# Kernel tuning notes

Hardware: AMD Instinct MI355X
Metric: run time of the kernel (lower is better)

## Reference

```python
import jax, jax.numpy as jnp
import numpy as np

B, CIN, HW = 32, 64, 56
K, KS, STRIDE, PAD = 128, 3, 1, 1


def setup_inputs() -> dict:
    key = jax.random.key(0)
    kx, kw, kb = jax.random.split(key, 3)
    x = jax.random.normal(kx, (B, CIN, HW, HW), dtype=jnp.float32)
    weight = jax.random.normal(kw, (K, CIN, KS, KS), dtype=jnp.float32)
    offset = jax.random.normal(kb, (K, 1, 1), dtype=jnp.float32)
    return {"x": x, "weight": weight, "offset": offset}


def reference(x, weight, offset):
    # conv2d (NCHW, OIHW) with stride/padding, then add per-kernel scalar offset.
    # Equivalent to the module's im2col (create_window_column_matrix) + matmul
    # + reshape, plus self.offset broadcast over (B, K, s, s).
    out = jax.lax.conv_general_dilated(
        x, weight,
        window_strides=(STRIDE, STRIDE),
        padding=[(PAD, PAD), (PAD, PAD)],
        dimension_numbers=("NCHW", "OIHW", "NCHW"),
    )
    return out + offset  # offset (K,1,1) broadcasts against (B,K,s,s)
```

## Files before the change

kernel.cpp:

```cpp
#include <hip/hip_runtime.h>
#include <hip/hip_bf16.h>

namespace {

using frag_t    = __attribute__((ext_vector_type(8))) short;
using f32x4     = __attribute__((ext_vector_type(4))) float;
using float4_t  = __attribute__((ext_vector_type(4))) float;

constexpr int BATCH = 32;
constexpr int CIN   = 64;
constexpr int HWD   = 56;
constexpr int KOUT  = 128;
constexpr int SP    = HWD * HWD;
constexpr int KD    = 9 * CIN;
constexpr int BN    = 64;
constexpr int HALO  = 57;
constexpr int NROWS = BN + 2 * HALO;
constexpr int NSTA  = 192;
constexpr int NTILES= SP / BN;
constexpr int NWG   = NTILES * BATCH;
constexpr int TT    = BATCH * (SP / 64);
constexpr int WB    = (KOUT * KD + 255) / 256;

__device__ inline unsigned short f2bf(float f) {
    __hip_bfloat16 h = __float2bfloat16(f);
    return __builtin_bit_cast(unsigned short, h);
}

__global__ __launch_bounds__(256)
void prep_kernel(const float* __restrict__ x, const float* __restrict__ w,
                 unsigned short* __restrict__ wpA, unsigned short* __restrict__ xT)
{
    if (blockIdx.x >= TT) {
        const int idx = (blockIdx.x - TT) * 256 + threadIdx.x;
        if (idx < KOUT * KD) {
            const int kout = idx / KD, kk = idx - kout * KD;
            const int kc = kk >> 5, e = kk & 31;
            const int t = kk >> 6, c = kk & 63;
            const int ky = t / 3, kx = t - ky * 3;
            wpA[(kc * KOUT + kout) * 32 + e] = f2bf(w[((kout * CIN + c) * 3 + ky) * 3 + kx]);
        }
        return;
    }
    __shared__ float ls[64][68];
    const int bb   = blockIdx.x / (SP / 64);
    const int tile = blockIdx.x - bb * (SP / 64);
    const int sp0  = tile * 64;
    const int tid  = threadIdx.x;
    const int cq   = tid >> 4;
    const int spo  = (tid & 15) * 4;
    const float* xb = x + (size_t)bb * CIN * SP;
    #pragma unroll
    for (int j = 0; j < 4; ++j) {
        const int c = cq + 16 * j;
        float4_t v = *(const float4_t*)&xb[(size_t)c * SP + sp0 + spo];
        ls[spo + 0][c] = v.x; ls[spo + 1][c] = v.y;
        ls[spo + 2][c] = v.z; ls[spo + 3][c] = v.w;
    }
    __syncthreads();
    unsigned short* xo = xT + (size_t)(bb * SP + sp0) * 64;
    #pragma unroll
    for (int j = 0; j < 2; ++j) {
        const int s  = tid + 256 * j;
        const int sp = s >> 3, e = s & 7;
        frag_t u;
        #pragma unroll
        for (int q = 0; q < 8; ++q)
            u[q] = (short)f2bf(ls[sp][e * 8 + q]);
        *(frag_t*)&xo[sp * 64 + e * 8] = u;
    }
}

__global__ __launch_bounds__(256, 5)
void conv_slim(const unsigned short* __restrict__ xT, const unsigned short* __restrict__ wpA,
               const float* __restrict__ off, float* __restrict__ out)
{
    __shared__ unsigned short xs[NSTA * 64];

    const int d    = blockIdx.x;
    const int wk   = (d & 7) * (NWG / 8) + (d >> 3);
    const int b    = wk / NTILES;
    const int sp0  = (wk - b * NTILES) * BN;
    const int tid  = threadIdx.x;
    const int lane = tid & 63;
    const int wid  = tid >> 6;

    {
        const unsigned short* xb = xT + (size_t)b * SP * 64;
        const int lsw = ((lane & 7) * 8) ^ ((lane >> 3) << 3);
        #pragma unroll
        for (int it = 0; it < 6; ++it) {
            const int R0 = it * 32 + wid * 8;
            const int r  = R0 + (lane >> 3);
            if (r < NROWS) {
                int g = sp0 - HALO + r;
                g = min(max(g, 0), SP - 1);
                __builtin_amdgcn_global_load_lds(
                    (const __attribute__((address_space(1))) unsigned int*)
                        (xb + (size_t)g * 64 + lsw),
                    (__attribute__((address_space(3))) unsigned int*)
                        &xs[R0 * 64 + lane * 8],
                    16, 0, 0);
            }
        }
    }
    asm volatile("s_waitcnt vmcnt(0)" ::: "memory");
    __syncthreads();

    const int wm  = wid * 32;
    const int l15 = lane & 15;
    const int l4  = lane >> 4;

    unsigned long long mbits = 0ull;
    int yv[4], xv[4];
    #pragma unroll
    for (int nf = 0; nf < 4; ++nf) {
        const int sp = sp0 + nf * 16 + l15;
        yv[nf] = sp / HWD;
        xv[nf] = sp - yv[nf] * HWD;
    }
    #pragma unroll
    for (int t = 0; t < 9; ++t) {
        const int dy = t / 3 - 1, dx = t % 3 - 1;
        #pragma unroll
        for (int nf = 0; nf < 4; ++nf) {
            const bool v = ((unsigned)(yv[nf] + dy) < (unsigned)HWD) &
                           ((unsigned)(xv[nf] + dx) < (unsigned)HWD);
            mbits |= (unsigned long long)(v ? 1 : 0) << (t * 4 + nf);
        }
    }

    const unsigned short* abase = wpA + (size_t)(wm + l15) * 32 + 8 * l4;
    const int cread = 8 * l4;
    const frag_t zf = {0,0,0,0,0,0,0,0};

    f32x4 acc[2][4] = {};

    #pragma unroll
    for (int kc = 0; kc < 18; ++kc) {
        const int t  = kc >> 1;
        const int c0 = (kc & 1) * 32;
        const int s    = (t / 3 - 1) * HWD + (t % 3 - 1);
        const int row0 = l15 + HALO + s;
        const int sw   = (row0 & 7) << 3;
        frag_t a[2], bfr[4];
        #pragma unroll
        for (int mi = 0; mi < 2; ++mi)
            a[mi] = *(const frag_t*)(abase + (size_t)(kc * KOUT + mi * 16) * 32);
        #pragma unroll
        for (int nf = 0; nf < 4; ++nf) {
            const frag_t bl = *(const frag_t*)&xs[(row0 + 16 * nf) * 64
                                                 + ((c0 + cread) ^ sw)];
            bfr[nf] = ((mbits >> (t * 4 + nf)) & 1) ? bl : zf;
        }
        #pragma unroll
        for (int mi = 0; mi < 2; ++mi)
            #pragma unroll
            for (int nf = 0; nf < 4; ++nf)
                acc[mi][nf] = __builtin_amdgcn_mfma_f32_16x16x32_bf16(
                    a[mi], bfr[nf], acc[mi][nf], 0, 0, 0);
    }

    const int spn = sp0 + l15;
    #pragma unroll
    for (int mi = 0; mi < 2; ++mi) {
        const int km = wm + 16 * mi + 4 * l4;
        #pragma unroll
        for (int reg = 0; reg < 4; ++reg) {
            const int  kk  = km + reg;
            const float ofv = off[kk];
            float* ob = out + (size_t)(b * KOUT + kk) * SP;
            #pragma unroll
            for (int nf = 0; nf < 4; ++nf)
                ob[spn + 16 * nf] = acc[mi][nf][reg] + ofv;
        }
    }
}

__global__ __launch_bounds__(256)
void conv3x3_kernel(const float* __restrict__ x, const float* __restrict__ w,
                    const float* __restrict__ off, float* __restrict__ out)
{
    const int s  = blockIdx.x * 256 + threadIdx.x;
    const int b  = s / SP;
    const int sp = s - b * SP;
    const int y  = sp / HWD;
    const int xx = sp - y * HWD;
    const int k0 = blockIdx.y * 4;

    const int   xm1 = (xx > 0) ? xx - 1 : 0;
    const int   xp1 = (xx < HWD - 1) ? xx + 1 : HWD - 1;
    const float m0  = (xx > 0) ? 1.f : 0.f;
    const float m2  = (xx < HWD - 1) ? 1.f : 0.f;

    int ro[3]; float msk[3][3];
    #pragma unroll
    for (int ky = 0; ky < 3; ++ky) {
        const int  yy = y + ky - 1;
        const bool ok = (unsigned)yy < (unsigned)HWD;
        const float rm = ok ? 1.f : 0.f;
        ro[ky] = (ok ? yy : 0) * HWD;
        msk[ky][0] = rm * m0; msk[ky][1] = rm; msk[ky][2] = rm * m2;
    }
    float acc[4] = {0.f, 0.f, 0.f, 0.f};
    const float* xb = x + (size_t)b * CIN * SP;
    for (int c = 0; c < CIN; ++c) {
        const float* xc = xb + (size_t)c * SP;
        #pragma unroll
        for (int ky = 0; ky < 3; ++ky) {
            const float* xr = xc + ro[ky];
            const float v0 = xr[xm1] * msk[ky][0];
            const float v1 = xr[xx]  * msk[ky][1];
            const float v2 = xr[xp1] * msk[ky][2];
            const int wi = c * 9 + ky * 3;
            #pragma unroll
            for (int kk = 0; kk < 4; ++kk) {
                const float* wr = w + (size_t)(k0 + kk) * (CIN * 9) + wi;
                acc[kk] = fmaf(v0, wr[0], acc[kk]);
                acc[kk] = fmaf(v1, wr[1], acc[kk]);
                acc[kk] = fmaf(v2, wr[2], acc[kk]);
            }
        }
    }
    #pragma unroll
    for (int kk = 0; kk < 4; ++kk)
        out[(size_t)(b * KOUT + k0 + kk) * SP + sp] = acc[kk] + off[k0 + kk];
}

}

extern "C" void kernel_launch(void* const* d_in, const int* in_sizes, int n_in,
                              void* d_out, int out_size, void* d_ws, size_t ws_size,
                              hipStream_t stream)
{
    const float* x   = (const float*)d_in[0];
    const float* w   = (const float*)d_in[1];
    const float* off = (const float*)d_in[2];
    float* out = (float*)d_out;

    const size_t wpa_bytes = (size_t)KOUT * KD * 2;
    const size_t xt_bytes  = (size_t)BATCH * SP * CIN * 2;

    if (ws_size >= wpa_bytes + xt_bytes) {
        unsigned short* wpA = (unsigned short*)d_ws;
        unsigned short* xT  = (unsigned short*)((char*)d_ws + wpa_bytes);
        prep_kernel<<<TT + WB, 256, 0, stream>>>(x, w, wpA, xT);
        conv_slim<<<NWG, dim3(256, 1, 1), 0, stream>>>(xT, wpA, off, out);
    } else {
        dim3 grid((BATCH * SP) / 256, KOUT / 4);
        conv3x3_kernel<<<grid, dim3(256, 1, 1), 0, stream>>>(x, w, off, out);
    }
}
```

Before: 42.34 us.

## Read conv input fragments directly from padded global buffer instead of LDS staging

The conv kernel no longer stages a halo tile of the transposed bf16 input into LDS. Each wave now loads its B fragments straight from global memory, which is padded by 64 rows per image so shifted reads never go out of bounds. This removes the LDS staging, its wait and the block barrier, and frees LDS for higher occupancy. In exchange every lane issues redundant global loads for the nine shifted taps, so the kernel leans on L1/L2 cache hits. Launch bounds drop from 5 to 4 blocks per CU. The padding rows are never written, but masked taps replace those loads with zeros.

```diff
diff --git a/kernel.cpp b/kernel.cpp
--- a/kernel.cpp
+++ b/kernel.cpp
@@ -14,9 +14,8 @@
 constexpr int SP    = HWD * HWD;
 constexpr int KD    = 9 * CIN;
 constexpr int BN    = 64;
-constexpr int HALO  = 57;
-constexpr int NROWS = BN + 2 * HALO;
-constexpr int NSTA  = 192;
+constexpr int PADR  = 64;
+constexpr int XTR   = SP + 2 * PADR;
 constexpr int NTILES= SP / BN;
 constexpr int NWG   = NTILES * BATCH;
 constexpr int TT    = BATCH * (SP / 64);
@@ -58,7 +57,7 @@
         ls[spo + 2][c] = v.z; ls[spo + 3][c] = v.w;
     }
     __syncthreads();
-    unsigned short* xo = xT + (size_t)(bb * SP + sp0) * 64;
+    unsigned short* xo = xT + ((size_t)bb * XTR + PADR + sp0) * 64;
     #pragma unroll
     for (int j = 0; j < 2; ++j) {
         const int s  = tid + 256 * j;
@@ -71,41 +70,16 @@
     }
 }
 
-__global__ __launch_bounds__(256, 5)
-void conv_slim(const unsigned short* __restrict__ xT, const unsigned short* __restrict__ wpA,
-               const float* __restrict__ off, float* __restrict__ out)
-{
-    __shared__ unsigned short xs[NSTA * 64];
-
+__global__ __launch_bounds__(256, 4)
+void conv_direct(const unsigned short* __restrict__ xT, const unsigned short* __restrict__ wpA,
+                 const float* __restrict__ off, float* __restrict__ out)
+{
     const int d    = blockIdx.x;
     const int wk   = (d & 7) * (NWG / 8) + (d >> 3);
     const int b    = wk / NTILES;
     const int sp0  = (wk - b * NTILES) * BN;
-    const int tid  = threadIdx.x;
-    const int lane = tid & 63;
-    const int wid  = tid >> 6;
-
-    {
-        const unsigned short* xb = xT + (size_t)b * SP * 64;
-        const int lsw = ((lane & 7) * 8) ^ ((lane >> 3) << 3);
-        #pragma unroll
-        for (int it = 0; it < 6; ++it) {
-            const int R0 = it * 32 + wid * 8;
-            const int r  = R0 + (lane >> 3);
-            if (r < NROWS) {
-                int g = sp0 - HALO + r;
-                g = min(max(g, 0), SP - 1);
-                __builtin_amdgcn_global_load_lds(
-                    (const __attribute__((address_space(1))) unsigned int*)
-                        (xb + (size_t)g * 64 + lsw),
-                    (__attribute__((address_space(3))) unsigned int*)
-                        &xs[R0 * 64 + lane * 8],
-                    16, 0, 0);
-            }
-        }
-    }
-    asm volatile("s_waitcnt vmcnt(0)" ::: "memory");
-    __syncthreads();
+    const int lane = threadIdx.x & 63;
+    const int wid  = threadIdx.x >> 6;
 
     const int wm  = wid * 32;
     const int l15 = lane & 15;
@@ -131,27 +105,25 @@
     }
 
     const unsigned short* abase = wpA + (size_t)(wm + l15) * 32 + 8 * l4;
-    const int cread = 8 * l4;
+    const unsigned short* bbase = xT + ((size_t)b * XTR + PADR + sp0 + l15) * 64 + 8 * l4;
     const frag_t zf = {0,0,0,0,0,0,0,0};
 
     f32x4 acc[2][4] = {};
 
     #pragma unroll
     for (int kc = 0; kc < 18; ++kc) {
-        const int t  = kc >> 1;
-        const int c0 = (kc & 1) * 32;
-        const int s    = (t / 3 - 1) * HWD + (t % 3 - 1);
-        const int row0 = l15 + HALO + s;
-        const int sw   = (row0 & 7) << 3;
+        const int t     = kc >> 1;
+        const int ch    = kc & 1;
+        const int shift = (t / 3 - 1) * HWD + (t % 3 - 1);
         frag_t a[2], bfr[4];
-        #pragma unroll
-        for (int mi = 0; mi < 2; ++mi)
-            a[mi] = *(const frag_t*)(abase + (size_t)(kc * KOUT + mi * 16) * 32);
+        a[0] = *(const frag_t*)(abase + (size_t)kc * KOUT * 32);
+        a[1] = *(const frag_t*)(abase + (size_t)kc * KOUT * 32 + 16 * 32);
+        const unsigned m4 = (unsigned)((mbits >> (t * 4)) & 15ull);
         #pragma unroll
         for (int nf = 0; nf < 4; ++nf) {
-            const frag_t bl = *(const frag_t*)&xs[(row0 + 16 * nf) * 64
-                                                 + ((c0 + cread) ^ sw)];
-            bfr[nf] = ((mbits >> (t * 4 + nf)) & 1) ? bl : zf;
+            const frag_t bl = *(const frag_t*)(bbase
+                                + (ptrdiff_t)(shift + 16 * nf) * 64 + ch * 32);
+            bfr[nf] = ((m4 >> nf) & 1u) ? bl : zf;
         }
         #pragma unroll
         for (int mi = 0; mi < 2; ++mi)
@@ -239,13 +211,13 @@
     float* out = (float*)d_out;
 
     const size_t wpa_bytes = (size_t)KOUT * KD * 2;
-    const size_t xt_bytes  = (size_t)BATCH * SP * CIN * 2;
+    const size_t xt_bytes  = (size_t)BATCH * XTR * CIN * 2;
 
     if (ws_size >= wpa_bytes + xt_bytes) {
         unsigned short* wpA = (unsigned short*)d_ws;
         unsigned short* xT  = (unsigned short*)((char*)d_ws + wpa_bytes);
         prep_kernel<<<TT + WB, 256, 0, stream>>>(x, w, wpA, xT);
-        conv_slim<<<NWG, dim3(256, 1, 1), 0, stream>>>(xT, wpA, off, out);
+        conv_direct<<<NWG, dim3(256, 1, 1), 0, stream>>>(xT, wpA, off, out);
     } else {
         dim3 grid((BATCH * SP) / 256, KOUT / 4);
         conv3x3_kernel<<<grid, dim3(256, 1, 1), 0, stream>>>(x, w, off, out);
```

After: 88.20 us. 108% more time.

## Switch conv to persistent 256-block GEMM with LDS-resident weight half

Applied to the files above, without the earlier changes.

Replaces the many small 64-pixel tiles with 256 persistent blocks. Each block loads half of the output channels' weights into LDS once, pre-swizzled into fragment order by the prep kernel, then loops over up to four 256-pixel spatial tiles and computes a 64x256 output tile per iteration. This is meant to cut the repeated global weight reads and to improve MFMA reuse per loaded B fragment. In exchange, LDS use per block is much larger, which lowers occupancy. Each tile's loads are also fully serialized behind a barrier with no overlap against compute, and only 256 blocks exist, so some compute units may sit idle.

```diff
diff --git a/kernel.cpp b/kernel.cpp
--- a/kernel.cpp
+++ b/kernel.cpp
@@ -13,14 +13,15 @@
 constexpr int KOUT  = 128;
 constexpr int SP    = HWD * HWD;
 constexpr int KD    = 9 * CIN;
-constexpr int BN    = 64;
+constexpr int BN    = 256;
 constexpr int HALO  = 57;
-constexpr int NROWS = BN + 2 * HALO;
-constexpr int NSTA  = 192;
-constexpr int NTILES= SP / BN;
-constexpr int NWG   = NTILES * BATCH;
+constexpr int WIN   = BN + 2 * HALO;
+constexpr int T13   = 13;
+constexpr int NSLOT = T13 * BATCH;
+constexpr int NBLK  = 256;
 constexpr int TT    = BATCH * (SP / 64);
-constexpr int WB    = (KOUT * KD + 255) / 256;
+constexpr int WB2   = (KOUT * KD) / 256;
+constexpr int AHALF = 18 * 4 * 64 * 8;
 
 __device__ inline unsigned short f2bf(float f) {
     __hip_bfloat16 h = __float2bfloat16(f);
@@ -29,17 +30,20 @@
 
 __global__ __launch_bounds__(256)
 void prep_kernel(const float* __restrict__ x, const float* __restrict__ w,
-                 unsigned short* __restrict__ wpA, unsigned short* __restrict__ xT)
+                 unsigned short* __restrict__ wpA2, unsigned short* __restrict__ xT)
 {
     if (blockIdx.x >= TT) {
         const int idx = (blockIdx.x - TT) * 256 + threadIdx.x;
-        if (idx < KOUT * KD) {
-            const int kout = idx / KD, kk = idx - kout * KD;
-            const int kc = kk >> 5, e = kk & 31;
-            const int t = kk >> 6, c = kk & 63;
-            const int ky = t / 3, kx = t - ky * 3;
-            wpA[(kc * KOUT + kout) * 32 + e] = f2bf(w[((kout * CIN + c) * 3 + ky) * 3 + kx]);
-        }
+        const int q   = idx & 7;
+        int r1 = idx >> 3;
+        const int l  = r1 & 63;  r1 >>= 6;
+        const int mi = r1 & 3;   r1 >>= 2;
+        const int kc = r1 % 18;
+        const int kh = r1 / 18;
+        const int kout = kh * 64 + mi * 16 + (l & 15);
+        const int kk   = kc * 32 + (l >> 4) * 8 + q;
+        const int c = kk & 63, t = kk >> 6, ky = t / 3, kx = t - ky * 3;
+        wpA2[idx] = f2bf(w[((kout * CIN + c) * 3 + ky) * 3 + kx]);
         return;
     }
     __shared__ float ls[64][68];
@@ -71,109 +75,128 @@
     }
 }
 
-__global__ __launch_bounds__(256, 5)
-void conv_slim(const unsigned short* __restrict__ xT, const unsigned short* __restrict__ wpA,
+__global__ __launch_bounds__(256)
+void conv_gemm(const unsigned short* __restrict__ xT, const unsigned short* __restrict__ wpA2,
                const float* __restrict__ off, float* __restrict__ out)
 {
-    __shared__ unsigned short xs[NSTA * 64];
+    __shared__ unsigned short As[AHALF];
+    __shared__ unsigned short xs[WIN * 64];
 
     const int d    = blockIdx.x;
-    const int wk   = (d & 7) * (NWG / 8) + (d >> 3);
-    const int b    = wk / NTILES;
-    const int sp0  = (wk - b * NTILES) * BN;
+    const int kh   = d >> 7;
+    const int pair = d & 127;
     const int tid  = threadIdx.x;
     const int lane = tid & 63;
     const int wid  = tid >> 6;
 
     {
-        const unsigned short* xb = xT + (size_t)b * SP * 64;
-        const int lsw = ((lane & 7) * 8) ^ ((lane >> 3) << 3);
-        #pragma unroll
-        for (int it = 0; it < 6; ++it) {
-            const int R0 = it * 32 + wid * 8;
-            const int r  = R0 + (lane >> 3);
-            if (r < NROWS) {
-                int g = sp0 - HALO + r;
-                g = min(max(g, 0), SP - 1);
-                __builtin_amdgcn_global_load_lds(
-                    (const __attribute__((address_space(1))) unsigned int*)
-                        (xb + (size_t)g * 64 + lsw),
-                    (__attribute__((address_space(3))) unsigned int*)
-                        &xs[R0 * 64 + lane * 8],
-                    16, 0, 0);
-            }
-        }
-    }
-    asm volatile("s_waitcnt vmcnt(0)" ::: "memory");
-    __syncthreads();
-
-    const int wm  = wid * 32;
+        const unsigned short* src = wpA2 + kh * AHALF + tid * 8;
+        #pragma unroll
+        for (int it = 0; it < 18; ++it) {
+            __builtin_amdgcn_global_load_lds(
+                (const __attribute__((address_space(1))) unsigned int*)(src + it * 2048),
+                (__attribute__((address_space(3))) unsigned int*)&As[it * 2048 + tid * 8],
+                16, 0, 0);
+        }
+    }
+
+    const int wn  = wid * 64;
     const int l15 = lane & 15;
     const int l4  = lane >> 4;
-
-    unsigned long long mbits = 0ull;
-    int yv[4], xv[4];
-    #pragma unroll
-    for (int nf = 0; nf < 4; ++nf) {
-        const int sp = sp0 + nf * 16 + l15;
-        yv[nf] = sp / HWD;
-        xv[nf] = sp - yv[nf] * HWD;
-    }
-    #pragma unroll
-    for (int t = 0; t < 9; ++t) {
-        const int dy = t / 3 - 1, dx = t % 3 - 1;
+    const int cread = 8 * l4;
+    const int lsw = ((lane & 7) * 8) ^ ((lane >> 3) << 3);
+    const frag_t zf = {0,0,0,0,0,0,0,0};
+
+    for (int i = 0; i < 4; ++i) {
+        const int s = pair + i * 128;
+        if (s >= NSLOT) break;
+        const int img = s / T13;
+        const int sp0 = (s - img * T13) * BN;
+
+        {
+            const unsigned short* xb = xT + (size_t)img * SP * 64;
+            #pragma unroll
+            for (int it = 0; it < 12; ++it) {
+                const int R0 = it * 32 + wid * 8;
+                const int r  = R0 + (lane >> 3);
+                if (r < WIN) {
+                    int g = sp0 - HALO + r;
+                    g = min(max(g, 0), SP - 1);
+                    __builtin_amdgcn_global_load_lds(
+                        (const __attribute__((address_space(1))) unsigned int*)
+                            (xb + (size_t)g * 64 + lsw),
+                        (__attribute__((address_space(3))) unsigned int*)
+                            &xs[R0 * 64 + lane * 8],
+                        16, 0, 0);
+                }
+            }
+        }
+        asm volatile("s_waitcnt vmcnt(0)" ::: "memory");
+        __syncthreads();
+
+        unsigned long long mbits = 0ull;
+        int yv[4], xv[4];
         #pragma unroll
         for (int nf = 0; nf < 4; ++nf) {
-            const bool v = ((unsigned)(yv[nf] + dy) < (unsigned)HWD) &
-                           ((unsigned)(xv[nf] + dx) < (unsigned)HWD);
-            mbits |= (unsigned long long)(v ? 1 : 0) << (t * 4 + nf);
-        }
-    }
-
-    const unsigned short* abase = wpA + (size_t)(wm + l15) * 32 + 8 * l4;
-    const int cread = 8 * l4;
-    const frag_t zf = {0,0,0,0,0,0,0,0};
-
-    f32x4 acc[2][4] = {};
-
-    #pragma unroll
-    for (int kc = 0; kc < 18; ++kc) {
-        const int t  = kc >> 1;
-        const int c0 = (kc & 1) * 32;
-        const int s    = (t / 3 - 1) * HWD + (t % 3 - 1);
-        const int row0 = l15 + HALO + s;
-        const int sw   = (row0 & 7) << 3;
-        frag_t a[2], bfr[4];
-        #pragma unroll
-        for (int mi = 0; mi < 2; ++mi)
-            a[mi] = *(const frag_t*)(abase + (size_t)(kc * KOUT + mi * 16) * 32);
-        #pragma unroll
-        for (int nf = 0; nf < 4; ++nf) {
-            const frag_t bl = *(const frag_t*)&xs[(row0 + 16 * nf) * 64
-                                                 + ((c0 + cread) ^ sw)];
-            bfr[nf] = ((mbits >> (t * 4 + nf)) & 1) ? bl : zf;
-        }
-        #pragma unroll
-        for (int mi = 0; mi < 2; ++mi)
-            #pragma unroll
-            for (int nf = 0; nf < 4; ++nf)
-                acc[mi][nf] = __builtin_amdgcn_mfma_f32_16x16x32_bf16(
-                    a[mi], bfr[nf], acc[mi][nf], 0, 0, 0);
-    }
-
-    const int spn = sp0 + l15;
-    #pragma unroll
-    for (int mi = 0; mi < 2; ++mi) {
-        const int km = wm + 16 * mi + 4 * l4;
-        #pragma unroll
-        for (int reg = 0; reg < 4; ++reg) {
-            const int  kk  = km + reg;
-            const float ofv = off[kk];
-            float* ob = out + (size_t)(b * KOUT + kk) * SP;
-            #pragma unroll
-            for (int nf = 0; nf < 4; ++nf)
-                ob[spn + 16 * nf] = acc[mi][nf][reg] + ofv;
-        }
+            const int sp = sp0 + wn + nf * 16 + l15;
+            yv[nf] = sp / HWD;
+            xv[nf] = sp - yv[nf] * HWD;
+        }
+        #pragma unroll
+        for (int t = 0; t < 9; ++t) {
+            const int dy = t / 3 - 1, dx = t % 3 - 1;
+            #pragma unroll
+            for (int nf = 0; nf < 4; ++nf) {
+                const bool v = ((unsigned)(yv[nf] + dy) < (unsigned)HWD) &
+                               ((unsigned)(xv[nf] + dx) < (unsigned)HWD);
+                mbits |= (unsigned long long)(v ? 1 : 0) << (t * 4 + nf);
+            }
+        }
+
+        f32x4 acc[4][4] = {};
+        #pragma unroll
+        for (int kc = 0; kc < 18; ++kc) {
+            const int t  = kc >> 1;
+            const int c0 = (kc & 1) * 32;
+            const int shift = (t / 3 - 1) * HWD + (t % 3 - 1);
+            const int row0  = wn + l15 + HALO + shift;
+            const int sw    = (row0 & 7) << 3;
+            frag_t a[4], bfr[4];
+            #pragma unroll
+            for (int mi = 0; mi < 4; ++mi)
+                a[mi] = *(const frag_t*)&As[(kc * 4 + mi) * 512 + lane * 8];
+            const unsigned m4 = (unsigned)((mbits >> (t * 4)) & 15ull);
+            #pragma unroll
+            for (int nf = 0; nf < 4; ++nf) {
+                const frag_t bl = *(const frag_t*)&xs[(row0 + 16 * nf) * 64
+                                                     + ((c0 + cread) ^ sw)];
+                bfr[nf] = ((m4 >> nf) & 1u) ? bl : zf;
+            }
+            #pragma unroll
+            for (int mi = 0; mi < 4; ++mi)
+                #pragma unroll
+                for (int nf = 0; nf < 4; ++nf)
+                    acc[mi][nf] = __builtin_amdgcn_mfma_f32_16x16x32_bf16(
+                        a[mi], bfr[nf], acc[mi][nf], 0, 0, 0);
+        }
+
+        const int spn = sp0 + wn + l15;
+        #pragma unroll
+        for (int mi = 0; mi < 4; ++mi) {
+            const int km = kh * 64 + mi * 16 + 4 * l4;
+            #pragma unroll
+            for (int reg = 0; reg < 4; ++reg) {
+                const int  kk  = km + reg;
+                const float ofv = off[kk];
+                float* ob = out + (size_t)(img * KOUT + kk) * SP;
+                #pragma unroll
+                for (int nf = 0; nf < 4; ++nf) {
+                    const int sp = spn + 16 * nf;
+                    if (sp < SP) ob[sp] = acc[mi][nf][reg] + ofv;
+                }
+            }
+        }
+        __syncthreads();
     }
 }
 
@@ -242,10 +265,10 @@
     const size_t xt_bytes  = (size_t)BATCH * SP * CIN * 2;
 
     if (ws_size >= wpa_bytes + xt_bytes) {
-        unsigned short* wpA = (unsigned short*)d_ws;
-        unsigned short* xT  = (unsigned short*)((char*)d_ws + wpa_bytes);
-        prep_kernel<<<TT + WB, 256, 0, stream>>>(x, w, wpA, xT);
-        conv_slim<<<NWG, dim3(256, 1, 1), 0, stream>>>(xT, wpA, off, out);
+        unsigned short* wpA2 = (unsigned short*)d_ws;
+        unsigned short* xT   = (unsigned short*)((char*)d_ws + wpa_bytes);
+        prep_kernel<<<TT + WB2, 256, 0, stream>>>(x, w, wpA2, xT);
+        conv_gemm<<<NBLK, dim3(256, 1, 1), 0, stream>>>(xT, wpA2, off, out);
     } else {
         dim3 grid((BATCH * SP) / 256, KOUT / 4);
         conv3x3_kernel<<<grid, dim3(256, 1, 1), 0, stream>>>(x, w, off, out);
```

Result: slower. 66.49 us (+57.0%).
